# Kernel tuning notes

Measured on AMD Instinct MI355X. Metric: run time of the kernel, lower is better.

Reference implementation:

```python
import jax, jax.numpy as jnp
import numpy as np

N_NODES = 100000
N_EDGES = 1600000
D = 128


def setup_inputs() -> dict:
    key = jax.random.key(0)
    ks = jax.random.split(key, 6)
    x = jax.random.normal(ks[0], (N_NODES, D), dtype=jnp.float32)
    src = jax.random.randint(ks[1], (N_EDGES,), 0, N_NODES, dtype=jnp.int32)
    dst = jax.random.randint(ks[2], (N_EDGES,), 0, N_NODES, dtype=jnp.int32)
    # Xavier-ish small weights
    W1 = jax.random.normal(ks[3], (D, D), dtype=jnp.float32) * 0.05
    W2 = jax.random.normal(ks[4], (D, D), dtype=jnp.float32) * 0.05
    b1 = jnp.zeros((D,), dtype=jnp.float32)
    b2 = jnp.zeros((D,), dtype=jnp.float32)
    prelu_a = jnp.full((1,), 0.25, dtype=jnp.float32)  # nn.PReLU default, shared across layers
    return {"x": x, "src": src, "dst": dst, "W1": W1, "b1": b1, "W2": W2, "b2": b2, "prelu_a": prelu_a}


def reference(x, src, dst, W1, b1, W2, b2, prelu_a):
    N = x.shape[0]
    # DGL GraphConv norm='left': scale source features by 1/clamp(out_degree, 1)
    deg = jax.ops.segment_sum(jnp.ones(src.shape, x.dtype), src, num_segments=N)
    inv_outdeg = (1.0 / jnp.maximum(deg, 1.0))[:, None]  # [N,1]

    def layer(h, W, b):
        h = h * inv_outdeg                                   # left-normalize sources
        agg = jax.ops.segment_sum(h[src], dst, num_segments=N)  # SpMM: sum messages at dst
        z = agg @ W + b                                      # dense transform (aggregate-first since in==out feats)
        return jnp.where(z >= 0, z, prelu_a * z)             # shared PReLU

    z = layer(x, W1, b1)
    z = layer(z, W2, b2)
    return z
```

## Files before the change

### kernel.cpp

```cpp
#include <hip/hip_runtime.h>

#define D 128
#define CAP 64
#define PADR 136

#define BSHIFT 7
#define NCH 256

typedef short short8 __attribute__((ext_vector_type(8)));
typedef float floatx4 __attribute__((ext_vector_type(4)));

static __device__ __forceinline__ unsigned short f2bf(float f) {
    unsigned int u = __float_as_uint(f);
    u += 0x7fffu + ((u >> 16) & 1u);
    return (unsigned short)(u >> 16);
}
static __device__ __forceinline__ unsigned int pack2bf(float a, float b) {
    return (unsigned int)f2bf(a) | ((unsigned int)f2bf(b) << 16);
}
static __device__ __forceinline__ int rd16(const unsigned int* __restrict__ pc, int v) {
    return (int)((pc[v >> 1] >> ((v & 1) * 16)) & 0xffffu);
}

__global__ __launch_bounds__(512) void k_cnt(const int* __restrict__ dst,
                                             unsigned int* __restrict__ gcnt,
                                             int E, int cs, int nbuck) {
    __shared__ unsigned int h[1024];
    int b = blockIdx.x, t = threadIdx.x;
    for (int k = t; k < nbuck; k += 512) h[k] = 0;
    __syncthreads();
    int lo = b * cs, hi = lo + cs;
    if (hi > E) hi = E;
#pragma unroll 4
    for (int e = lo + t; e < hi; e += 512)
        atomicAdd(&h[(unsigned)dst[e] >> BSHIFT], 1u);
    __syncthreads();
    for (int k = t; k < nbuck; k += 512) gcnt[(size_t)b * nbuck + k] = h[k];
}

__global__ __launch_bounds__(NCH) void k_pfx1(unsigned int* __restrict__ gcnt,
                                              unsigned int* __restrict__ btot, int nbuck) {
    __shared__ unsigned int sa[NCH], sb[NCH];
    int k = blockIdx.x, t = threadIdx.x;
    unsigned int v = gcnt[(size_t)t * nbuck + k];
    sa[t] = v;
    unsigned int* A = sa; unsigned int* B = sb;
    for (int off = 1; off < NCH; off <<= 1) {
        __syncthreads();
        B[t] = A[t] + ((t >= off) ? A[t - off] : 0u);
        unsigned int* tmp = A; A = B; B = tmp;
    }
    __syncthreads();
    unsigned int incl = A[t];
    gcnt[(size_t)t * nbuck + k] = incl - v;
    if (t == NCH - 1) btot[k] = incl;
}

__global__ __launch_bounds__(1024) void k_pfx2(const unsigned int* __restrict__ btot,
                                               unsigned int* __restrict__ bstart,
                                               int nbuck, int E) {
    __shared__ unsigned int sa[1024], sb[1024];
    int t = threadIdx.x;
    unsigned int v = (t < nbuck) ? btot[t] : 0u;
    sa[t] = v;
    unsigned int* A = sa; unsigned int* B = sb;
    for (int off = 1; off < 1024; off <<= 1) {
        __syncthreads();
        B[t] = A[t] + ((t >= off) ? A[t - off] : 0u);
        unsigned int* tmp = A; A = B; B = tmp;
    }
    __syncthreads();
    if (t < nbuck) bstart[t] = A[t] - v;
    if (t == 0) bstart[nbuck] = (unsigned int)E;
}

__global__ __launch_bounds__(512) void k_scat(const int* __restrict__ src, const int* __restrict__ dst,
                                              const unsigned int* __restrict__ goff,
                                              const unsigned int* __restrict__ bstart,
                                              unsigned int* __restrict__ pcnt_out,
                                              unsigned int* __restrict__ bdata,
                                              int E, int cs, int nbuck) {
    __shared__ unsigned int cur[1024];
    int b = blockIdx.x, t = threadIdx.x;
    for (int k = t; k < nbuck; k += 512)
        cur[k] = bstart[k] + goff[(size_t)b * nbuck + k];
    __syncthreads();
    int lo = b * cs, hi = lo + cs;
    if (hi > E) hi = E;
#pragma unroll 2
    for (int e = lo + t; e < hi; e += 512) {
        int s = src[e];
        int d = dst[e];
        atomicAdd(&pcnt_out[s >> 1], 1u << ((s & 1) * 16));
        unsigned int p = atomicAdd(&cur[(unsigned)d >> BSHIFT], 1u);
        bdata[p] = ((unsigned int)(d & 127) << 17) | (unsigned int)s;
    }
}

__global__ __launch_bounds__(256) void k_csr(
    const unsigned int* __restrict__ bdata, const unsigned int* __restrict__ bstart,
    unsigned int* __restrict__ pcnt_in, int* __restrict__ esrc, int n) {
    __shared__ unsigned int lcnt[128];
    int b = blockIdx.x;
    int base = b << BSHIFT;
    if (threadIdx.x < 128) lcnt[threadIdx.x] = 0;
    __syncthreads();
    int lo = (int)bstart[b], hi = (int)bstart[b + 1];
    for (int i = lo + threadIdx.x; i < hi; i += 256) {
        unsigned int e = bdata[i];
        int s = (int)(e & 0x1FFFFu);
        int dl = (int)(e >> 17);
        unsigned int p = atomicAdd(&lcnt[dl], 1u);
        if (p < CAP) esrc[((size_t)(base + dl) << 6) + p] = s;
    }
    __syncthreads();
    if (threadIdx.x < 64) {
        int node0 = base + threadIdx.x * 2;
        if (node0 < n) {
            unsigned int c0 = lcnt[threadIdx.x * 2];
            unsigned int c1 = lcnt[threadIdx.x * 2 + 1];
            pcnt_in[(base >> 1) + threadIdx.x] = (c0 & 0xffffu) | (c1 << 16);
        }
    }
}

__global__ void k_prep(const float* __restrict__ x, const unsigned int* __restrict__ pcnt_out,
                       float* __restrict__ inv, uint2* __restrict__ xb2, int total4,
                       const float* __restrict__ W1, const float* __restrict__ W2,
                       unsigned short* __restrict__ WT1, unsigned short* __restrict__ WT2) {
    int b = blockIdx.x;
    int nb4 = (total4 + 255) >> 8;
    if (b >= nb4) {
        int bb = b - nb4;
        const float* W = (bb < 64) ? W1 : W2;
        unsigned short* WT = (bb < 64) ? WT1 : WT2;
        int idx = (bb & 63) * 256 + threadIdx.x;
        int k = idx >> 7, nn = idx & 127;
        WT[nn * 128 + k] = f2bf(W[idx]);
        return;
    }
    int i = b * 256 + threadIdx.x;
    if (i >= total4) return;
    int row = i >> 5;
    int d = rd16(pcnt_out, row);
    float s = 1.0f / (float)(d > 1 ? d : 1);
    if ((i & 31) == 0) inv[row] = s;
    float4 v = ((const float4*)x)[i];
    uint2 o;
    o.x = pack2bf(v.x * s, v.y * s);
    o.y = pack2bf(v.z * s, v.w * s);
    xb2[i] = o;
}

template<bool OUTBF>
__global__ __launch_bounds__(256) void k_fused(
    const uint4* __restrict__ hb4, const unsigned int* __restrict__ pcnt_in,
    const int* __restrict__ esrc, const unsigned short* __restrict__ WT,
    const float* __restrict__ bias, const float* __restrict__ pa,
    const float* __restrict__ inv, void* __restrict__ outp, int n)
{
    __shared__ unsigned short sAgg[16 * PADR];
    int wv = threadIdx.x >> 6;
    int lane = threadIdx.x & 63;
    int q = lane >> 4;
    int f = lane & 15;
    int nb = blockIdx.x * 16;

    for (int i = 0; i < 4; i++) {
        int node = nb + wv * 4 + i;
        if (node >= n) break;
        int cnt = rd16(pcnt_in, node);
        if (cnt > CAP) cnt = CAP;
        const int* ep = esrc + (node << 6);

        float acc[8];
#pragma unroll
        for (int j = 0; j < 8; j++) acc[j] = 0.f;

        for (int base = 0; base < cnt; base += 8) {
            int e0 = base + q, e1 = base + 4 + q;
            if (e0 < cnt) {
                uint4 v = hb4[(size_t)ep[e0] * 16 + f];
                acc[0] += __uint_as_float(v.x << 16);  acc[1] += __uint_as_float(v.x & 0xffff0000u);
                acc[2] += __uint_as_float(v.y << 16);  acc[3] += __uint_as_float(v.y & 0xffff0000u);
                acc[4] += __uint_as_float(v.z << 16);  acc[5] += __uint_as_float(v.z & 0xffff0000u);
                acc[6] += __uint_as_float(v.w << 16);  acc[7] += __uint_as_float(v.w & 0xffff0000u);
            }
            if (e1 < cnt) {
                uint4 v = hb4[(size_t)ep[e1] * 16 + f];
                acc[0] += __uint_as_float(v.x << 16);  acc[1] += __uint_as_float(v.x & 0xffff0000u);
                acc[2] += __uint_as_float(v.y << 16);  acc[3] += __uint_as_float(v.y & 0xffff0000u);
                acc[4] += __uint_as_float(v.z << 16);  acc[5] += __uint_as_float(v.z & 0xffff0000u);
                acc[6] += __uint_as_float(v.w << 16);  acc[7] += __uint_as_float(v.w & 0xffff0000u);
            }
        }
#pragma unroll
        for (int j = 0; j < 8; j++) {
            acc[j] += __shfl_xor(acc[j], 16, 64);
            acc[j] += __shfl_xor(acc[j], 32, 64);
        }
        if (q == 0) {
            uint4 o;
            o.x = pack2bf(acc[0], acc[1]);
            o.y = pack2bf(acc[2], acc[3]);
            o.z = pack2bf(acc[4], acc[5]);
            o.w = pack2bf(acc[6], acc[7]);
            *(uint4*)&sAgg[(wv * 4 + i) * PADR + f * 8] = o;
        }
    }
    __syncthreads();

    int m = lane & 15;
    short8 a0 = *(const short8*)&sAgg[m * PADR +   0 + q * 8];
    short8 a1 = *(const short8*)&sAgg[m * PADR +  32 + q * 8];
    short8 a2 = *(const short8*)&sAgg[m * PADR +  64 + q * 8];
    short8 a3 = *(const short8*)&sAgg[m * PADR +  96 + q * 8];

    float alpha = pa[0];
    float* outf = (float*)outp;
    unsigned short* outb = (unsigned short*)outp;

    float invr[4];
    if (OUTBF) {
#pragma unroll
        for (int r = 0; r < 4; r++) {
            int row = nb + q * 4 + r;
            invr[r] = (row < n) ? inv[row] : 1.f;
        }
    }

#pragma unroll
    for (int tt = 0; tt < 2; tt++) {
        int t = wv * 2 + tt;
        int col = t * 16 + m;
        const short8* Bp = (const short8*)(WT + (size_t)col * 128 + q * 8);
        floatx4 acc = {0.f, 0.f, 0.f, 0.f};
        acc = __builtin_amdgcn_mfma_f32_16x16x32_bf16(a0, Bp[0],  acc, 0, 0, 0);
        acc = __builtin_amdgcn_mfma_f32_16x16x32_bf16(a1, Bp[4],  acc, 0, 0, 0);
        acc = __builtin_amdgcn_mfma_f32_16x16x32_bf16(a2, Bp[8],  acc, 0, 0, 0);
        acc = __builtin_amdgcn_mfma_f32_16x16x32_bf16(a3, Bp[12], acc, 0, 0, 0);
        float bb = bias[col];
#pragma unroll
        for (int r = 0; r < 4; r++) {
            int row = nb + q * 4 + r;
            if (row < n) {
                float z = acc[r] + bb;
                z = (z >= 0.f) ? z : alpha * z;
                if (OUTBF)
                    outb[(size_t)row * 128 + col] = f2bf(z * invr[r]);
                else
                    outf[(size_t)row * 128 + col] = z;
            }
        }
    }
}

__global__ __launch_bounds__(256) void k_gather(
    const uint4* __restrict__ hb4, const unsigned int* __restrict__ pcnt_in,
    const int* __restrict__ esrc, uint4* __restrict__ aggb4, int n)
{
    int lane = threadIdx.x & 63;
    int node = blockIdx.x * 4 + (threadIdx.x >> 6);
    if (node >= n) return;
    int q = lane >> 4, f = lane & 15;
    int cnt = rd16(pcnt_in, node);
    if (cnt > CAP) cnt = CAP;
    const int* ep = esrc + (node << 6);

    float acc[8];
#pragma unroll
    for (int j = 0; j < 8; j++) acc[j] = 0.f;

    for (int base = 0; base < cnt; base += 8) {
        int e0 = base + q, e1 = base + 4 + q;
        if (e0 < cnt) {
            uint4 v = hb4[(size_t)ep[e0] * 16 + f];
            acc[0] += __uint_as_float(v.x << 16);  acc[1] += __uint_as_float(v.x & 0xffff0000u);
            acc[2] += __uint_as_float(v.y << 16);  acc[3] += __uint_as_float(v.y & 0xffff0000u);
            acc[4] += __uint_as_float(v.z << 16);  acc[5] += __uint_as_float(v.z & 0xffff0000u);
            acc[6] += __uint_as_float(v.w << 16);  acc[7] += __uint_as_float(v.w & 0xffff0000u);
        }
        if (e1 < cnt) {
            uint4 v = hb4[(size_t)ep[e1] * 16 + f];
            acc[0] += __uint_as_float(v.x << 16);  acc[1] += __uint_as_float(v.x & 0xffff0000u);
            acc[2] += __uint_as_float(v.y << 16);  acc[3] += __uint_as_float(v.y & 0xffff0000u);
            acc[4] += __uint_as_float(v.z << 16);  acc[5] += __uint_as_float(v.z & 0xffff0000u);
            acc[6] += __uint_as_float(v.w << 16);  acc[7] += __uint_as_float(v.w & 0xffff0000u);
        }
    }
#pragma unroll
    for (int j = 0; j < 8; j++) {
        acc[j] += __shfl_xor(acc[j], 16, 64);
        acc[j] += __shfl_xor(acc[j], 32, 64);
    }
    if (q == 0) {
        uint4 o;
        o.x = pack2bf(acc[0], acc[1]);
        o.y = pack2bf(acc[2], acc[3]);
        o.z = pack2bf(acc[4], acc[5]);
        o.w = pack2bf(acc[6], acc[7]);
        aggb4[(size_t)node * 16 + f] = o;
    }
}

__global__ __launch_bounds__(256) void k_gemm(
    const unsigned short* __restrict__ A, const unsigned short* __restrict__ WT,
    const float* __restrict__ bias, const float* __restrict__ pa,
    float* __restrict__ outf, int n)
{
    int lane = threadIdx.x & 63;
    int wv = threadIdx.x >> 6;
    int m = lane & 15, q = lane >> 4;
    int mbase = blockIdx.x * 64 + wv * 16;
    int arow = mbase + m;
    if (arow > n - 1) arow = n - 1;

    const short8* Ap = (const short8*)(A + (size_t)arow * 128 + q * 8);
    short8 a0 = Ap[0], a1 = Ap[4], a2 = Ap[8], a3 = Ap[12];

    float alpha = pa[0];
#pragma unroll
    for (int t = 0; t < 8; t++) {
        int col = t * 16 + m;
        const short8* Bp = (const short8*)(WT + (size_t)col * 128 + q * 8);
        floatx4 acc = {0.f, 0.f, 0.f, 0.f};
        acc = __builtin_amdgcn_mfma_f32_16x16x32_bf16(a0, Bp[0],  acc, 0, 0, 0);
        acc = __builtin_amdgcn_mfma_f32_16x16x32_bf16(a1, Bp[4],  acc, 0, 0, 0);
        acc = __builtin_amdgcn_mfma_f32_16x16x32_bf16(a2, Bp[8],  acc, 0, 0, 0);
        acc = __builtin_amdgcn_mfma_f32_16x16x32_bf16(a3, Bp[12], acc, 0, 0, 0);
        float bb = bias[col];
#pragma unroll
        for (int r = 0; r < 4; r++) {
            int row = mbase + q * 4 + r;
            if (row < n) {
                float z = acc[r] + bb;
                z = (z >= 0.f) ? z : alpha * z;
                outf[(size_t)row * 128 + col] = z;
            }
        }
    }
}

extern "C" void kernel_launch(void* const* d_in, const int* in_sizes, int n_in,
                              void* d_out, int out_size, void* d_ws, size_t ws_size,
                              hipStream_t stream) {
    const float* x   = (const float*)d_in[0];
    const int* src   = (const int*)d_in[1];
    const int* dst   = (const int*)d_in[2];
    const float* W1  = (const float*)d_in[3];
    const float* b1  = (const float*)d_in[4];
    const float* W2  = (const float*)d_in[5];
    const float* b2  = (const float*)d_in[6];
    const float* pa  = (const float*)d_in[7];
    float* out = (float*)d_out;

    const int N = in_sizes[0] / D;
    const int E = in_sizes[1];

    char* ws = (char*)d_ws;
    size_t off = 0;
    unsigned short* buf0 = (unsigned short*)(ws + off); off += (size_t)N * D * 2;
    unsigned short* buf1 = (unsigned short*)(ws + off); off += (size_t)N * D * 2;
    unsigned int* pcnt_out = (unsigned int*)(ws + off); off += (size_t)((N + 1) / 2) * 4;
    unsigned int* pcnt_in  = (unsigned int*)(ws + off); off += (size_t)((N + 1) / 2) * 4;
    float* inv   = (float*)(ws + off); off += (size_t)N * sizeof(float);
    unsigned short* WT1 = (unsigned short*)(ws + off); off += 128 * 128 * 2;
    unsigned short* WT2 = (unsigned short*)(ws + off); off += 128 * 128 * 2;
    size_t off_esrc = off;
    size_t need_big = off_esrc + (size_t)N * CAP * sizeof(int);
    bool big = (ws_size >= need_big);

    int* esrc = big ? (int*)(ws + off_esrc) : (int*)d_out;

    const int nbuck = (N + (1 << BSHIFT) - 1) >> BSHIFT;
    unsigned int* bdata  = (unsigned int*)buf1;
    unsigned int* gcnt   = bdata + E;
    unsigned int* btot   = gcnt + (size_t)NCH * nbuck;
    unsigned int* bstart = btot + nbuck;

    hipMemsetAsync(pcnt_out, 0, (size_t)((N + 1) / 2) * 4, stream);

    const int cs = (E + NCH - 1) / NCH;
    k_cnt <<<NCH, 512, 0, stream>>>(dst, gcnt, E, cs, nbuck);
    k_pfx1<<<nbuck, NCH, 0, stream>>>(gcnt, btot, nbuck);
    k_pfx2<<<1, 1024, 0, stream>>>(btot, bstart, nbuck, E);
    k_scat<<<NCH, 512, 0, stream>>>(src, dst, gcnt, bstart, pcnt_out, bdata, E, cs, nbuck);
    k_csr <<<nbuck, 256, 0, stream>>>(bdata, bstart, pcnt_in, esrc, N);

    const int total4 = N * (D / 4);
    const int NBP = (total4 + 255) / 256 + 128;
    k_prep<<<NBP, 256, 0, stream>>>(x, pcnt_out, inv, (uint2*)buf0, total4, W1, W2, WT1, WT2);

    const int NBF = (N + 15) / 16;

    k_fused<true><<<NBF, 256, 0, stream>>>((const uint4*)buf0, pcnt_in, esrc, WT1, b1, pa, inv,
                                           (void*)buf1, N);

    if (big) {
        k_fused<false><<<NBF, 256, 0, stream>>>((const uint4*)buf1, pcnt_in, esrc, WT2, b2, pa, inv,
                                                (void*)out, N);
    } else {
        const int NBG = (N + 3) / 4;
        const int NBM = (N + 63) / 64;
        k_gather<<<NBG, 256, 0, stream>>>((const uint4*)buf1, pcnt_in, esrc, (uint4*)buf0, N);
        k_gemm<<<NBM, 256, 0, stream>>>(buf0, WT2, b2, pa, out, N);
    }
}
```

Baseline: 396.2 us.

## Pad edge lists to multiples of eight with zero row, batch gathers two nodes

Each node's edge list is padded up to a multiple of eight entries that point at an extra all-zero feature row, appended to both bf16 buffers and zeroed in the prep kernel. The aggregation loops then drop their per-edge bounds checks, load two source indices per lane as an int2, and each wave processes two destination nodes at a time so more independent gathers are in flight. The final fp32 output store becomes nontemporal. In exchange, padded entries add wasted gathers of the zero row, and the workspace layout shifts by one row.

```diff
diff --git a/kernel.cpp b/kernel.cpp
--- a/kernel.cpp
+++ b/kernel.cpp
@@ -20,6 +20,12 @@
 }
 static __device__ __forceinline__ int rd16(const unsigned int* __restrict__ pc, int v) {
     return (int)((pc[v >> 1] >> ((v & 1) * 16)) & 0xffffu);
+}
+static __device__ __forceinline__ void acc8(float* a, uint4 v) {
+    a[0] += __uint_as_float(v.x << 16);  a[1] += __uint_as_float(v.x & 0xffff0000u);
+    a[2] += __uint_as_float(v.y << 16);  a[3] += __uint_as_float(v.y & 0xffff0000u);
+    a[4] += __uint_as_float(v.z << 16);  a[5] += __uint_as_float(v.z & 0xffff0000u);
+    a[6] += __uint_as_float(v.w << 16);  a[7] += __uint_as_float(v.w & 0xffff0000u);
 }
 
 __global__ __launch_bounds__(512) void k_cnt(const int* __restrict__ dst,
@@ -114,6 +120,16 @@
         if (p < CAP) esrc[((size_t)(base + dl) << 6) + p] = s;
     }
     __syncthreads();
+    if (threadIdx.x < 128) {
+        int node = base + threadIdx.x;
+        if (node < n) {
+            int c = (int)lcnt[threadIdx.x];
+            if (c > CAP) c = CAP;
+            int cp = (c + 7) & ~7;
+            for (int p = c; p < cp; p++)
+                esrc[((size_t)node << 6) + p] = n;
+        }
+    }
     if (threadIdx.x < 64) {
         int node0 = base + threadIdx.x * 2;
         if (node0 < n) {
@@ -127,9 +143,15 @@
 __global__ void k_prep(const float* __restrict__ x, const unsigned int* __restrict__ pcnt_out,
                        float* __restrict__ inv, uint2* __restrict__ xb2, int total4,
                        const float* __restrict__ W1, const float* __restrict__ W2,
-                       unsigned short* __restrict__ WT1, unsigned short* __restrict__ WT2) {
+                       unsigned short* __restrict__ WT1, unsigned short* __restrict__ WT2,
+                       uint4* __restrict__ z0, uint4* __restrict__ z1) {
     int b = blockIdx.x;
     int nb4 = (total4 + 255) >> 8;
+    if (b >= nb4 + 128) {
+        if (threadIdx.x < 16) z0[threadIdx.x] = (uint4){0u, 0u, 0u, 0u};
+        else if (threadIdx.x < 32) z1[threadIdx.x - 16] = (uint4){0u, 0u, 0u, 0u};
+        return;
+    }
     if (b >= nb4) {
         int bb = b - nb4;
         const float* W = (bb < 64) ? W1 : W2;
@@ -166,46 +188,47 @@
     int f = lane & 15;
     int nb = blockIdx.x * 16;
 
-    for (int i = 0; i < 4; i++) {
-        int node = nb + wv * 4 + i;
-        if (node >= n) break;
-        int cnt = rd16(pcnt_in, node);
-        if (cnt > CAP) cnt = CAP;
-        const int* ep = esrc + (node << 6);
-
-        float acc[8];
-#pragma unroll
-        for (int j = 0; j < 8; j++) acc[j] = 0.f;
-
-        for (int base = 0; base < cnt; base += 8) {
-            int e0 = base + q, e1 = base + 4 + q;
-            if (e0 < cnt) {
-                uint4 v = hb4[(size_t)ep[e0] * 16 + f];
-                acc[0] += __uint_as_float(v.x << 16);  acc[1] += __uint_as_float(v.x & 0xffff0000u);
-                acc[2] += __uint_as_float(v.y << 16);  acc[3] += __uint_as_float(v.y & 0xffff0000u);
-                acc[4] += __uint_as_float(v.z << 16);  acc[5] += __uint_as_float(v.z & 0xffff0000u);
-                acc[6] += __uint_as_float(v.w << 16);  acc[7] += __uint_as_float(v.w & 0xffff0000u);
-            }
-            if (e1 < cnt) {
-                uint4 v = hb4[(size_t)ep[e1] * 16 + f];
-                acc[0] += __uint_as_float(v.x << 16);  acc[1] += __uint_as_float(v.x & 0xffff0000u);
-                acc[2] += __uint_as_float(v.y << 16);  acc[3] += __uint_as_float(v.y & 0xffff0000u);
-                acc[4] += __uint_as_float(v.z << 16);  acc[5] += __uint_as_float(v.z & 0xffff0000u);
-                acc[6] += __uint_as_float(v.w << 16);  acc[7] += __uint_as_float(v.w & 0xffff0000u);
-            }
+    for (int ii = 0; ii < 4; ii += 2) {
+        int nodeA = nb + wv * 4 + ii;
+        int nodeB = nodeA + 1;
+        int cA = (nodeA < n) ? rd16(pcnt_in, nodeA) : 0;
+        int cB = (nodeB < n) ? rd16(pcnt_in, nodeB) : 0;
+        if (cA > CAP) cA = CAP;
+        if (cB > CAP) cB = CAP;
+        cA = (cA + 7) & ~7;
+        cB = (cB + 7) & ~7;
+        const int* epA = esrc + ((size_t)nodeA << 6);
+        const int* epB = esrc + ((size_t)nodeB << 6);
+        float accA[8], accB[8];
+#pragma unroll
+        for (int j = 0; j < 8; j++) { accA[j] = 0.f; accB[j] = 0.f; }
+        int mx = cA > cB ? cA : cB;
+        for (int base = 0; base < mx; base += 8) {
+            bool dA = base < cA, dB = base < cB;
+            int2 eA, eB;
+            uint4 vA0, vA1, vB0, vB1;
+            if (dA) eA = *(const int2*)(epA + base + 2 * q);
+            if (dB) eB = *(const int2*)(epB + base + 2 * q);
+            if (dA) { vA0 = hb4[(size_t)eA.x * 16 + f]; vA1 = hb4[(size_t)eA.y * 16 + f]; }
+            if (dB) { vB0 = hb4[(size_t)eB.x * 16 + f]; vB1 = hb4[(size_t)eB.y * 16 + f]; }
+            if (dA) { acc8(accA, vA0); acc8(accA, vA1); }
+            if (dB) { acc8(accB, vB0); acc8(accB, vB1); }
         }
 #pragma unroll
         for (int j = 0; j < 8; j++) {
-            acc[j] += __shfl_xor(acc[j], 16, 64);
-            acc[j] += __shfl_xor(acc[j], 32, 64);
+            accA[j] += __shfl_xor(accA[j], 16, 64);
+            accA[j] += __shfl_xor(accA[j], 32, 64);
+            accB[j] += __shfl_xor(accB[j], 16, 64);
+            accB[j] += __shfl_xor(accB[j], 32, 64);
         }
         if (q == 0) {
-            uint4 o;
-            o.x = pack2bf(acc[0], acc[1]);
-            o.y = pack2bf(acc[2], acc[3]);
-            o.z = pack2bf(acc[4], acc[5]);
-            o.w = pack2bf(acc[6], acc[7]);
-            *(uint4*)&sAgg[(wv * 4 + i) * PADR + f * 8] = o;
+            uint4 oA, oB;
+            oA.x = pack2bf(accA[0], accA[1]); oA.y = pack2bf(accA[2], accA[3]);
+            oA.z = pack2bf(accA[4], accA[5]); oA.w = pack2bf(accA[6], accA[7]);
+            oB.x = pack2bf(accB[0], accB[1]); oB.y = pack2bf(accB[2], accB[3]);
+            oB.z = pack2bf(accB[4], accB[5]); oB.w = pack2bf(accB[6], accB[7]);
+            if (nodeA < n) *(uint4*)&sAgg[(wv * 4 + ii) * PADR + f * 8] = oA;
+            if (nodeB < n) *(uint4*)&sAgg[(wv * 4 + ii + 1) * PADR + f * 8] = oB;
         }
     }
     __syncthreads();
@@ -249,7 +272,7 @@
                 if (OUTBF)
                     outb[(size_t)row * 128 + col] = f2bf(z * invr[r]);
                 else
-                    outf[(size_t)row * 128 + col] = z;
+                    __builtin_nontemporal_store(z, &outf[(size_t)row * 128 + col]);
             }
         }
     }
@@ -265,28 +288,19 @@
     int q = lane >> 4, f = lane & 15;
     int cnt = rd16(pcnt_in, node);
     if (cnt > CAP) cnt = CAP;
-    const int* ep = esrc + (node << 6);
+    cnt = (cnt + 7) & ~7;
+    const int* ep = esrc + ((size_t)node << 6);
 
     float acc[8];
 #pragma unroll
     for (int j = 0; j < 8; j++) acc[j] = 0.f;
 
     for (int base = 0; base < cnt; base += 8) {
-        int e0 = base + q, e1 = base + 4 + q;
-        if (e0 < cnt) {
-            uint4 v = hb4[(size_t)ep[e0] * 16 + f];
-            acc[0] += __uint_as_float(v.x << 16);  acc[1] += __uint_as_float(v.x & 0xffff0000u);
-            acc[2] += __uint_as_float(v.y << 16);  acc[3] += __uint_as_float(v.y & 0xffff0000u);
-            acc[4] += __uint_as_float(v.z << 16);  acc[5] += __uint_as_float(v.z & 0xffff0000u);
-            acc[6] += __uint_as_float(v.w << 16);  acc[7] += __uint_as_float(v.w & 0xffff0000u);
-        }
-        if (e1 < cnt) {
-            uint4 v = hb4[(size_t)ep[e1] * 16 + f];
-            acc[0] += __uint_as_float(v.x << 16);  acc[1] += __uint_as_float(v.x & 0xffff0000u);
-            acc[2] += __uint_as_float(v.y << 16);  acc[3] += __uint_as_float(v.y & 0xffff0000u);
-            acc[4] += __uint_as_float(v.z << 16);  acc[5] += __uint_as_float(v.z & 0xffff0000u);
-            acc[6] += __uint_as_float(v.w << 16);  acc[7] += __uint_as_float(v.w & 0xffff0000u);
-        }
+        int2 e = *(const int2*)(ep + base + 2 * q);
+        uint4 v0 = hb4[(size_t)e.x * 16 + f];
+        uint4 v1 = hb4[(size_t)e.y * 16 + f];
+        acc8(acc, v0);
+        acc8(acc, v1);
     }
 #pragma unroll
     for (int j = 0; j < 8; j++) {
@@ -359,8 +373,8 @@
 
     char* ws = (char*)d_ws;
     size_t off = 0;
-    unsigned short* buf0 = (unsigned short*)(ws + off); off += (size_t)N * D * 2;
-    unsigned short* buf1 = (unsigned short*)(ws + off); off += (size_t)N * D * 2;
+    unsigned short* buf0 = (unsigned short*)(ws + off); off += (size_t)(N + 1) * D * 2;
+    unsigned short* buf1 = (unsigned short*)(ws + off); off += (size_t)(N + 1) * D * 2;
     unsigned int* pcnt_out = (unsigned int*)(ws + off); off += (size_t)((N + 1) / 2) * 4;
     unsigned int* pcnt_in  = (unsigned int*)(ws + off); off += (size_t)((N + 1) / 2) * 4;
     float* inv   = (float*)(ws + off); off += (size_t)N * sizeof(float);
@@ -388,8 +402,10 @@
     k_csr <<<nbuck, 256, 0, stream>>>(bdata, bstart, pcnt_in, esrc, N);
 
     const int total4 = N * (D / 4);
-    const int NBP = (total4 + 255) / 256 + 128;
-    k_prep<<<NBP, 256, 0, stream>>>(x, pcnt_out, inv, (uint2*)buf0, total4, W1, W2, WT1, WT2);
+    const int NBP = (total4 + 255) / 256 + 128 + 1;
+    uint4* z0 = (uint4*)(buf0 + (size_t)N * D);
+    uint4* z1 = (uint4*)(buf1 + (size_t)N * D);
+    k_prep<<<NBP, 256, 0, stream>>>(x, pcnt_out, inv, (uint2*)buf0, total4, W1, W2, WT1, WT2, z0, z1);
 
     const int NBF = (N + 15) / 16;
 
```

After: 379.7 us. -4.2%, faster.
